# Kernel tuning notes

Measured on AMD Instinct MI355X. Metric: run time of the kernel, lower is better.

Reference implementation:

```python
import jax, jax.numpy as jnp
import numpy as np

N0, N1, N2 = 16000, 12000, 6000
K0, K1 = 10, 5
H, OUT = 256, 128
VOCABS = [50000, 1000, 200]
EDIMS = [64, 32, 32]
EIN = sum(EDIMS)  # 128 input to fc_input


def setup_inputs() -> dict:
    key = jax.random.key(0)
    ks = jax.random.split(key, 40)
    inp = {}
    cols = [jax.random.randint(ks[i], (N0, 1), 0, VOCABS[i]) for i in range(3)]
    inp['x'] = jnp.concatenate(cols, axis=1)
    inp['idx_sim0'] = jax.random.randint(ks[3], (N1, K0), 0, N0)
    inp['idx_cor0'] = jax.random.randint(ks[4], (N1, K0), 0, N0)
    inp['idx_sim1'] = jax.random.randint(ks[5], (N2, K1), 0, N1)
    inp['idx_cor1'] = jax.random.randint(ks[6], (N2, K1), 0, N1)
    k = 7
    for m in ['sim', 'cor']:
        for i in range(3):
            inp[f'emb{i}_{m}'] = jax.random.normal(ks[k], (VOCABS[i], EDIMS[i]), jnp.float32) * 0.02; k += 1
        inp[f'Win_{m}'] = jax.random.normal(ks[k], (EIN, H), jnp.float32) * (1.0 / np.sqrt(EIN)); k += 1
        inp[f'bin_{m}'] = jnp.zeros((H,), jnp.float32)
        inp[f'Wout_{m}'] = jax.random.normal(ks[k], (H, OUT), jnp.float32) * (1.0 / np.sqrt(H)); k += 1
        inp[f'bout_{m}'] = jnp.zeros((OUT,), jnp.float32)
    inp['Ws2c'] = jax.random.normal(ks[k], (OUT, OUT), jnp.float32) * (1.0 / np.sqrt(OUT)); k += 1
    inp['Wc2s'] = jax.random.normal(ks[k], (OUT, OUT), jnp.float32) * (1.0 / np.sqrt(OUT)); k += 1
    inp['a1'] = jnp.array([0.3], jnp.float32)
    inp['a2'] = jnp.array([0.25], jnp.float32)
    inp['b2'] = jnp.array([0.2], jnp.float32)
    return inp


def _coattention(D, Q):
    # D, Q: [N, K, H]
    L = jnp.einsum('nkh,nmh->nkm', D, Q)          # [N, K, K]
    AC = jax.nn.softmax(L, axis=-1)
    AS = jax.nn.softmax(jnp.swapaxes(L, 1, 2), axis=-1)
    CQ = jnp.einsum('nkm,nmh->nkh', AC, Q)        # [N, K, H]
    CD = jnp.einsum('nkm,nmh->nkh', AS, jnp.concatenate([D, CQ], axis=-1))  # [N, K, 2H]
    return jnp.concatenate([Q, CD], axis=-1)       # [N, K, 3H]


def _coagg(feat, idx_sim, idx_cor, mode, n_dst):
    # gather neighbor features per dst node (feat_src[in_edges_id])
    if mode == 'cor':
        D, Q = feat[idx_sim], feat[idx_cor]
    else:
        D, Q = feat[idx_cor], feat[idx_sim]
    h = _coattention(D, Q)                         # [n_dst, K, 3H]
    n, k, f = h.shape
    # AvgPool1d(kernel=3, stride=3) over feature axis -> [n_dst, K, H]
    pooled = h.reshape(n, k, f // 3, 3).mean(axis=-1)
    neigh = pooled.mean(axis=1)                    # mean over neighbors -> [n_dst, H]
    return feat[:n_dst] + neigh


def _branch(x, e0, e1, e2, Win, bin_, Wout, bout, i_s0, i_c0, i_s1, i_c1, mode):
    e = jnp.concatenate([e0[x[:, 0]], e1[x[:, 1]], e2[x[:, 2]]], axis=1)  # [N0, 128]
    h = e @ Win + bin_                             # [N0, H]
    h = jax.nn.relu(_coagg(h, i_s0, i_c0, mode, N1))
    h = _coagg(h, i_s1, i_c1, mode, N2)
    return h @ Wout + bout                         # [N2, OUT]


def reference(x, idx_sim0, idx_cor0, idx_sim1, idx_cor1,
              emb0_sim, emb1_sim, emb2_sim, Win_sim, bin_sim, Wout_sim, bout_sim,
              emb0_cor, emb1_cor, emb2_cor, Win_cor, bin_cor, Wout_cor, bout_cor,
              Ws2c, Wc2s, a1, a2, b2):
    sim = _branch(x, emb0_sim, emb1_sim, emb2_sim, Win_sim, bin_sim, Wout_sim, bout_sim,
                  idx_sim0, idx_cor0, idx_sim1, idx_cor1, 'sim')
    cor = _branch(x, emb0_cor, emb1_cor, emb2_cor, Win_cor, bin_cor, Wout_cor, bout_cor,
                  idx_sim0, idx_cor0, idx_sim1, idx_cor1, 'cor')
    # SemanticIntegration
    z1sim = (1 - a1) * sim + a1 * (cor @ Wc2s)
    z1cor = (1 - a1) * cor + a1 * (sim @ Ws2c)
    z2sim = (1 - a2 - b2) * sim + a2 * (cor @ Wc2s) + b2 * (z1cor @ Wc2s)
    z2cor = (1 - a2 - b2) * cor + a2 * (sim @ Ws2c) + b2 * (z1sim @ Ws2c)
    return jnp.stack([z2sim, z2cor])               # [2, N2, OUT]
```

## Files before the change

### kernel.cpp

```cpp
#include <hip/hip_runtime.h>

#define CH 256

template <int CTRL>
__device__ __forceinline__ float dppAdd(float v) {
    const int m = __builtin_amdgcn_update_dpp(0, __builtin_bit_cast(int, v), CTRL, 0xf, 0xf, true);
    return v + __builtin_bit_cast(float, m);
}

#define OPAQUE4(v) asm volatile("" : "+v"((v).x), "+v"((v).y), "+v"((v).z), "+v"((v).w))

__global__ __launch_bounds__(256) void embed_fc2_kernel(
    const int* __restrict__ x,
    const float* __restrict__ e0a, const float* __restrict__ e1a, const float* __restrict__ e2a,
    const float* __restrict__ Wina, const float* __restrict__ bina, float* __restrict__ h0a,
    const float* __restrict__ e0b, const float* __restrict__ e1b, const float* __restrict__ e2b,
    const float* __restrict__ Winb, const float* __restrict__ binb, float* __restrict__ h0b,
    const int blocksPer)
{
    __shared__ __align__(16) float eT[128][32];
    int bid = blockIdx.x;
    const float *e0, *e1, *e2, *Win, *bin;
    float* h0;
    if (bid < blocksPer) { e0 = e0a; e1 = e1a; e2 = e2a; Win = Wina; bin = bina; h0 = h0a; }
    else { bid -= blocksPer; e0 = e0b; e1 = e1b; e2 = e2b; Win = Winb; bin = binb; h0 = h0b; }

    const int row0 = bid * 32;
    const int t = threadIdx.x;
    const int w = t >> 6, l = t & 63;
    const int r = l & 31;
    const int kcBase = 2 * w + (l >> 5);

#pragma unroll
    for (int j = 0; j < 4; ++j) {
        const int kc = kcBase + 8 * j;
        const int k0 = kc * 4;
        const int row = row0 + r;
        float4 v;
        if (kc < 16)      v = *(const float4*)(e0 + (size_t)x[row * 3 + 0] * 64 + k0);
        else if (kc < 24) v = *(const float4*)(e1 + (size_t)x[row * 3 + 1] * 32 + (k0 - 64));
        else              v = *(const float4*)(e2 + (size_t)x[row * 3 + 2] * 32 + (k0 - 96));
        eT[k0 + 0][r] = v.x; eT[k0 + 1][r] = v.y; eT[k0 + 2][r] = v.z; eT[k0 + 3][r] = v.w;
    }
    __syncthreads();

    const float4 bb = *(const float4*)(bin + l * 4);
    float acc[8][4];
#pragma unroll
    for (int rr = 0; rr < 8; ++rr) {
        acc[rr][0] = bb.x; acc[rr][1] = bb.y; acc[rr][2] = bb.z; acc[rr][3] = bb.w;
    }
#pragma unroll 4
    for (int k = 0; k < 128; ++k) {
        const float4 wv = *(const float4*)(Win + (size_t)k * 256 + l * 4);
        const float4 ea = *(const float4*)&eT[k][w * 8];
        const float4 eb = *(const float4*)&eT[k][w * 8 + 4];
        const float ev[8] = {ea.x, ea.y, ea.z, ea.w, eb.x, eb.y, eb.z, eb.w};
#pragma unroll
        for (int rr = 0; rr < 8; ++rr) {
            acc[rr][0] += ev[rr] * wv.x; acc[rr][1] += ev[rr] * wv.y;
            acc[rr][2] += ev[rr] * wv.z; acc[rr][3] += ev[rr] * wv.w;
        }
    }
#pragma unroll
    for (int rr = 0; rr < 8; ++rr) {
        float4 o = make_float4(acc[rr][0], acc[rr][1], acc[rr][2], acc[rr][3]);
        *(float4*)(h0 + (size_t)(row0 + w * 8 + rr) * 256 + l * 4) = o;
    }
}

template <int KD, int MODE>
__global__ __launch_bounds__(128) void gemm16_kernel(
    const float* __restrict__ ina, const float* __restrict__ Wa,
    const float* __restrict__ auxa, const float* __restrict__ aux2a, float* __restrict__ oa,
    const float* __restrict__ inb, const float* __restrict__ Wb,
    const float* __restrict__ auxb, const float* __restrict__ aux2b, float* __restrict__ ob,
    const int blocksPer, const int nRows,
    const float* __restrict__ a1p, const float* __restrict__ a2p, const float* __restrict__ b2p)
{
    __shared__ __align__(16) float inT[KD][16];
    int bid = blockIdx.x;
    const float *in, *W, *aux, *aux2; float* outp;
    if (bid < blocksPer) { in = ina; W = Wa; aux = auxa; aux2 = aux2a; outp = oa; }
    else { bid -= blocksPer; in = inb; W = Wb; aux = auxb; aux2 = aux2b; outp = ob; }

    const int row0 = bid * 16;
    const int t = threadIdx.x;
    const int row = t & 15;
    const int kc0 = t >> 4;

#pragma unroll
    for (int j = 0; j < KD / 32; ++j) {
        const int kc = kc0 + 8 * j;
        const int k0 = kc * 4;
        int r = row0 + row;
        if (r >= nRows) r = nRows - 1;
        const float4 v = *(const float4*)(in + (size_t)r * KD + k0);
        inT[k0 + 0][row] = v.x; inT[k0 + 1][row] = v.y;
        inT[k0 + 2][row] = v.z; inT[k0 + 3][row] = v.w;
    }
    __syncthreads();

    const int w = t >> 6, l = t & 63;
    const int rg = w * 2 + (l >> 5);
    const int r0 = rg * 4;
    const int cc0 = (l & 31) * 4;

    float acc[4][4];
    if constexpr (MODE == 0) {
        const float4 bb = *(const float4*)(aux + cc0);
#pragma unroll
        for (int rr = 0; rr < 4; ++rr) {
            acc[rr][0] = bb.x; acc[rr][1] = bb.y; acc[rr][2] = bb.z; acc[rr][3] = bb.w;
        }
    } else {
#pragma unroll
        for (int rr = 0; rr < 4; ++rr) acc[rr][0] = acc[rr][1] = acc[rr][2] = acc[rr][3] = 0.f;
    }

#pragma unroll 4
    for (int k = 0; k < KD; ++k) {
        const float4 wv = *(const float4*)(W + (size_t)k * 128 + cc0);
        const float4 ea = *(const float4*)&inT[k][r0];
        const float ev[4] = {ea.x, ea.y, ea.z, ea.w};
#pragma unroll
        for (int rr = 0; rr < 4; ++rr) {
            acc[rr][0] += ev[rr] * wv.x; acc[rr][1] += ev[rr] * wv.y;
            acc[rr][2] += ev[rr] * wv.z; acc[rr][3] += ev[rr] * wv.w;
        }
    }

    float c0 = 0.f, c1 = 0.f, c2 = 0.f;
    if constexpr (MODE == 1) {
        const float a1 = *a1p, a2 = *a2p, b2 = *b2p;
        c0 = 1.f - a2 - b2;
        c1 = a2 + b2 * (1.f - a1);
        c2 = b2 * a1;
    }

#pragma unroll
    for (int rr = 0; rr < 4; ++rr) {
        const int r = row0 + r0 + rr;
        if (r < nRows) {
            float4 o = make_float4(acc[rr][0], acc[rr][1], acc[rr][2], acc[rr][3]);
            if constexpr (MODE == 1) {
                const size_t idx = (size_t)r * 128 + cc0;
                const float4 b1v = *(const float4*)(aux + idx);
                const float4 b2v = *(const float4*)(aux2 + idx);
                o.x = c0 * b1v.x + c1 * b2v.x + c2 * o.x;
                o.y = c0 * b1v.y + c1 * b2v.y + c2 * o.y;
                o.z = c0 * b1v.z + c1 * b2v.z + c2 * o.z;
                o.w = c0 * b1v.w + c1 * b2v.w + c2 * o.w;
            }
            *(float4*)(outp + (size_t)r * 128 + cc0) = o;
        }
    }
}

template <int K>
__global__ __launch_bounds__(256, 2) void coagg_kernel(
    const float* __restrict__ fa, const int* __restrict__ iDa, const int* __restrict__ iQa,
    float* __restrict__ oa,
    const float* __restrict__ fb, const int* __restrict__ iDb, const int* __restrict__ iQb,
    float* __restrict__ ob,
    const int nPer, const int relu)
{
    __shared__ float sL[4][K][K];
    __shared__ float sAC[4][K][K];
    __shared__ float sAS[4][K][K];
    __shared__ float sw_[4][K], su_[4][K];
    __shared__ __align__(16) float sHsum[4][768];

    const int t = threadIdx.x;
    const int wv = t >> 6, lane = t & 63;
    int n = blockIdx.x * 4 + wv;

    const float* feat; const int* idxD; const int* idxQ; float* outp;
    if (n < nPer) { feat = fa; idxD = iDa; idxQ = iQa; outp = oa; }
    else { n -= nPer; feat = fb; idxD = iDb; idxQ = iQb; outp = ob; }

    const float4* fp = (const float4*)feat;

    float4 d[K], q[K];
#pragma unroll
    for (int k = 0; k < K; ++k) {
        const int rD = idxD[n * K + k];
        const int rQ = idxQ[n * K + k];
        d[k] = fp[(size_t)rD * 64 + lane];
        q[k] = fp[(size_t)rQ * 64 + lane];
    }
    const float4 resid = fp[(size_t)n * 64 + lane];
#pragma unroll
    for (int k = 0; k < K; ++k) { OPAQUE4(d[k]); OPAQUE4(q[k]); }

#pragma unroll
    for (int k = 0; k < K; ++k) {
        const float4 dd = d[k];
#pragma unroll
        for (int m0 = 0; m0 < K; m0 += 4) {
            const float4 q0 = q[m0];
            float s0 = dd.x * q0.x + dd.y * q0.y + dd.z * q0.z + dd.w * q0.w;
            float s1 = 0.f, s2 = 0.f, s3 = 0.f;
            if (m0 + 1 < K) {
                const float4 qq = q[(m0 + 1 < K) ? m0 + 1 : 0];
                s1 = dd.x * qq.x + dd.y * qq.y + dd.z * qq.z + dd.w * qq.w;
            }
            if (m0 + 2 < K) {
                const float4 qq = q[(m0 + 2 < K) ? m0 + 2 : 0];
                s2 = dd.x * qq.x + dd.y * qq.y + dd.z * qq.z + dd.w * qq.w;
            }
            if (m0 + 3 < K) {
                const float4 qq = q[(m0 + 3 < K) ? m0 + 3 : 0];
                s3 = dd.x * qq.x + dd.y * qq.y + dd.z * qq.z + dd.w * qq.w;
            }
            asm volatile("v_permlane32_swap_b32 %0, %1" : "+v"(s0), "+v"(s1));
            float a = s0 + s1;
            asm volatile("v_permlane32_swap_b32 %0, %1" : "+v"(s2), "+v"(s3));
            float b = s2 + s3;
            asm volatile("v_permlane16_swap_b32 %0, %1" : "+v"(a), "+v"(b));
            float r = a + b;
            r = dppAdd<0x111>(r);
            r = dppAdd<0x112>(r);
            r = dppAdd<0x114>(r);
            r = dppAdd<0x118>(r);
            const int rowid = lane >> 4;
            const int mm = m0 + (((rowid & 1) << 1) | (rowid >> 1));
            if ((lane & 15) == 15 && mm < K) sL[wv][k][mm] = r;
        }
    }

    if (lane < K) {
        float e_[K], mx = -1e30f;
#pragma unroll
        for (int m = 0; m < K; ++m) mx = fmaxf(mx, sL[wv][lane][m]);
        float ssum = 0.f;
#pragma unroll
        for (int m = 0; m < K; ++m) { e_[m] = __expf(sL[wv][lane][m] - mx); ssum += e_[m]; }
        const float inv = 1.f / ssum;
#pragma unroll
        for (int m = 0; m < K; ++m) sAC[wv][lane][m] = e_[m] * inv;
    }
    {
        const int c = lane - 16;
        if (c >= 0 && c < K) {
            float e_[K], mx = -1e30f;
#pragma unroll
            for (int m = 0; m < K; ++m) mx = fmaxf(mx, sL[wv][m][c]);
            float ssum = 0.f;
#pragma unroll
            for (int m = 0; m < K; ++m) { e_[m] = __expf(sL[wv][m][c] - mx); ssum += e_[m]; }
            const float inv = 1.f / ssum;
#pragma unroll
            for (int m = 0; m < K; ++m) sAS[wv][c][m] = e_[m] * inv;
        }
    }
    {
        const int m2 = lane - 32;
        if (m2 >= 0 && m2 < K) {
            float s = 0.f;
#pragma unroll
            for (int k2 = 0; k2 < K; ++k2) s += sAS[wv][k2][m2];
            sw_[wv][m2] = s;
        }
    }
    {
        const int j2 = lane - 48;
        if (j2 >= 0 && j2 < K) {
            float s = 0.f;
#pragma unroll
            for (int m = 0; m < K; ++m) s += sw_[wv][m] * sAC[wv][m][j2];
            su_[wv][j2] = s;
        }
    }

    float4 h0v = make_float4(0.f, 0.f, 0.f, 0.f);
    float4 h1v = make_float4(0.f, 0.f, 0.f, 0.f);
    float4 h2v = make_float4(0.f, 0.f, 0.f, 0.f);
#pragma unroll
    for (int kx = 0; kx < K; ++kx) {
        const float wk = sw_[wv][kx];
        const float uk = su_[wv][kx];
        const float4 qq = q[kx];
        const float4 dd = d[kx];
        h0v.x += qq.x;      h0v.y += qq.y;      h0v.z += qq.z;      h0v.w += qq.w;
        h1v.x += wk * dd.x; h1v.y += wk * dd.y; h1v.z += wk * dd.z; h1v.w += wk * dd.w;
        h2v.x += uk * qq.x; h2v.y += uk * qq.y; h2v.z += uk * qq.z; h2v.w += uk * qq.w;
    }
    ((float4*)&sHsum[wv][0])[lane]       = h0v;
    ((float4*)&sHsum[wv][0])[64 + lane]  = h1v;
    ((float4*)&sHsum[wv][0])[128 + lane] = h2v;

    float ov[4];
#pragma unroll
    for (int i = 0; i < 4; ++i) {
        const int f = lane * 4 + i;
        ov[i] = (sHsum[wv][3 * f] + sHsum[wv][3 * f + 1] + sHsum[wv][3 * f + 2])
                * (1.0f / (3.0f * K));
    }
    float4 o = make_float4(resid.x + ov[0], resid.y + ov[1],
                           resid.z + ov[2], resid.w + ov[3]);
    if (relu) {
        o.x = fmaxf(o.x, 0.f); o.y = fmaxf(o.y, 0.f);
        o.z = fmaxf(o.z, 0.f); o.w = fmaxf(o.w, 0.f);
    }
    ((float4*)outp)[(size_t)n * 64 + lane] = o;
}

extern "C" void kernel_launch(void* const* d_in, const int* in_sizes, int n_in,
                              void* d_out, int out_size, void* d_ws, size_t ws_size,
                              hipStream_t stream)
{
    const int* x        = (const int*)d_in[0];
    const int* idx_sim0 = (const int*)d_in[1];
    const int* idx_cor0 = (const int*)d_in[2];
    const int* idx_sim1 = (const int*)d_in[3];
    const int* idx_cor1 = (const int*)d_in[4];
    const float* e0s  = (const float*)d_in[5];
    const float* e1s  = (const float*)d_in[6];
    const float* e2s  = (const float*)d_in[7];
    const float* Wins = (const float*)d_in[8];
    const float* bins = (const float*)d_in[9];
    const float* Wouts= (const float*)d_in[10];
    const float* bouts= (const float*)d_in[11];
    const float* e0c  = (const float*)d_in[12];
    const float* e1c  = (const float*)d_in[13];
    const float* e2c  = (const float*)d_in[14];
    const float* Winc = (const float*)d_in[15];
    const float* binc = (const float*)d_in[16];
    const float* Woutc= (const float*)d_in[17];
    const float* boutc= (const float*)d_in[18];
    const float* Ws2c = (const float*)d_in[19];
    const float* Wc2s = (const float*)d_in[20];
    const float* a1 = (const float*)d_in[21];
    const float* a2 = (const float*)d_in[22];
    const float* b2 = (const float*)d_in[23];

    float* outSim = (float*)d_out;
    float* outCor = outSim + 6000 * 128;

    float* ws = (float*)d_ws;
    const size_t needMerged = (size_t)(2 * 16000 * 256 + 2 * 12000 * 256 + 2 * 6000 * 256 + 4 * 6000 * 128) * 4;
    const bool merged = ws_size >= needMerged;

    const int fcBlocks = 6000 / 16;

    if (merged) {
        float* A0 = ws;
        float* A1 = A0 + 16000 * 256;
        float* B0 = A1 + 16000 * 256;
        float* B1 = B0 + 12000 * 256;
        float* C0 = B1 + 12000 * 256;
        float* C1 = C0 + 6000 * 256;
        float* simO = C1 + 6000 * 256;
        float* corO = simO + 6000 * 128;
        float* P    = corO + 6000 * 128;
        float* S    = P + 6000 * 128;

        embed_fc2_kernel<<<1000, 256, 0, stream>>>(x,
            e0s, e1s, e2s, Wins, bins, A0,
            e0c, e1c, e2c, Winc, binc, A1, 500);
        coagg_kernel<10><<<6000, 256, 0, stream>>>(
            A0, idx_cor0, idx_sim0, B0,
            A1, idx_sim0, idx_cor0, B1, 12000, 1);
        coagg_kernel<5><<<3000, 256, 0, stream>>>(
            B0, idx_cor1, idx_sim1, C0,
            B1, idx_sim1, idx_cor1, C1, 6000, 0);
        gemm16_kernel<256, 0><<<2 * fcBlocks, 128, 0, stream>>>(
            C0, Wouts, bouts, nullptr, simO,
            C1, Woutc, boutc, nullptr, corO, fcBlocks, 6000, a1, a2, b2);
        gemm16_kernel<128, 2><<<2 * fcBlocks, 128, 0, stream>>>(
            corO, Wc2s, nullptr, nullptr, P,
            simO, Ws2c, nullptr, nullptr, S, fcBlocks, 6000, a1, a2, b2);
        gemm16_kernel<128, 1><<<2 * fcBlocks, 128, 0, stream>>>(
            S, Wc2s, simO, P, outSim,
            P, Ws2c, corO, S, outCor, fcBlocks, 6000, a1, a2, b2);
    } else {
        float* A = ws;
        float* B = A + 16000 * 256;
        float* C = B + 12000 * 256;
        float* simO = C + 6000 * 256;
        float* corO = simO + 6000 * 128;
        float* P    = corO + 6000 * 128;
        float* S    = P + 6000 * 128;

        for (int b = 0; b < 2; ++b) {
            const float* e0   = (b == 0) ? e0s : e0c;
            const float* e1   = (b == 0) ? e1s : e1c;
            const float* e2   = (b == 0) ? e2s : e2c;
            const float* Win  = (b == 0) ? Wins : Winc;
            const float* bin  = (b == 0) ? bins : binc;
            const float* Wout = (b == 0) ? Wouts : Woutc;
            const float* bout = (b == 0) ? bouts : boutc;
            const int* iD0 = (b == 0) ? idx_cor0 : idx_sim0;
            const int* iQ0 = (b == 0) ? idx_sim0 : idx_cor0;
            const int* iD1 = (b == 0) ? idx_cor1 : idx_sim1;
            const int* iQ1 = (b == 0) ? idx_sim1 : idx_cor1;
            float* branchOut = (b == 0) ? simO : corO;

            embed_fc2_kernel<<<500, 256, 0, stream>>>(x,
                e0, e1, e2, Win, bin, A,
                e0, e1, e2, Win, bin, A, 500);
            coagg_kernel<10><<<3000, 256, 0, stream>>>(
                A, iD0, iQ0, B, A, iD0, iQ0, B, 12000, 1);
            coagg_kernel<5><<<1500, 256, 0, stream>>>(
                B, iD1, iQ1, C, B, iD1, iQ1, C, 6000, 0);
            gemm16_kernel<256, 0><<<fcBlocks, 128, 0, stream>>>(
                C, Wout, bout, nullptr, branchOut,
                C, Wout, bout, nullptr, branchOut, fcBlocks, 6000, a1, a2, b2);
        }
        gemm16_kernel<128, 2><<<2 * fcBlocks, 128, 0, stream>>>(
            corO, Wc2s, nullptr, nullptr, P,
            simO, Ws2c, nullptr, nullptr, S, fcBlocks, 6000, a1, a2, b2);
        gemm16_kernel<128, 1><<<2 * fcBlocks, 128, 0, stream>>>(
            S, Wc2s, simO, P, outSim,
            P, Ws2c, corO, S, outCor, fcBlocks, 6000, a1, a2, b2);
    }
}
```

Measured before the change: 176.0 us.

## Fold output FC and semantic integration into precomputed combined weight matrices

Algebraically composes Wout with Ws2c/Wc2s and the mixing coefficients into combined 256x128 weight matrices and biases, computed by two small prep kernels. The three tail GEMM launches (output FC, cross projection, final mix) become one fused kernel that reads C0 and C1 once and writes both outputs. This removes the intermediate simO/corO/P/S round trips and two launches, at the cost of two extra tiny launches and different floating-point rounding order.

Measured after the change: 215.3 us. 1.22x slower.

```diff
diff --git a/kernel.cpp b/kernel.cpp
--- a/kernel.cpp
+++ b/kernel.cpp
@@ -154,6 +154,206 @@
             }
             *(float4*)(outp + (size_t)r * 128 + cc0) = o;
         }
+    }
+}
+
+__global__ __launch_bounds__(128) void prep1_kernel(
+    const float* __restrict__ Ws2c, const float* __restrict__ Wc2s,
+    const float* __restrict__ bouts, const float* __restrict__ boutc,
+    float* __restrict__ Msc, float* __restrict__ Mcs,
+    float* __restrict__ vs, float* __restrict__ vc)
+{
+    const int bid = blockIdx.x;
+    const int t = threadIdx.x;
+    if (bid == 16) {
+        float s1 = 0.f, s2 = 0.f;
+        for (int k = 0; k < 128; ++k) {
+            s1 += bouts[k] * Ws2c[k * 128 + t];
+            s2 += boutc[k] * Wc2s[k * 128 + t];
+        }
+        vs[t] = s1; vc[t] = s2;
+        return;
+    }
+    const bool isSc = bid < 8;
+    const float* A = isSc ? Ws2c : Wc2s;
+    const float* W = isSc ? Wc2s : Ws2c;
+    float* out = isSc ? Msc : Mcs;
+    const int row0 = (bid & 7) * 16;
+
+    __shared__ __align__(16) float aT[128][16];
+    const int row = t & 15, kc0 = t >> 4;
+#pragma unroll
+    for (int j = 0; j < 4; ++j) {
+        const int k0 = (kc0 + 8 * j) * 4;
+        const float4 v = *(const float4*)(A + (size_t)(row0 + row) * 128 + k0);
+        aT[k0 + 0][row] = v.x; aT[k0 + 1][row] = v.y;
+        aT[k0 + 2][row] = v.z; aT[k0 + 3][row] = v.w;
+    }
+    __syncthreads();
+    const int w = t >> 6, l = t & 63;
+    const int r0 = (w * 2 + (l >> 5)) * 4;
+    const int cc0 = (l & 31) * 4;
+    float acc[4][4];
+#pragma unroll
+    for (int rr = 0; rr < 4; ++rr) acc[rr][0] = acc[rr][1] = acc[rr][2] = acc[rr][3] = 0.f;
+#pragma unroll 4
+    for (int k = 0; k < 128; ++k) {
+        const float4 wv = *(const float4*)(W + (size_t)k * 128 + cc0);
+        const float4 ea = *(const float4*)&aT[k][r0];
+        const float ev[4] = {ea.x, ea.y, ea.z, ea.w};
+#pragma unroll
+        for (int rr = 0; rr < 4; ++rr) {
+            acc[rr][0] += ev[rr] * wv.x; acc[rr][1] += ev[rr] * wv.y;
+            acc[rr][2] += ev[rr] * wv.z; acc[rr][3] += ev[rr] * wv.w;
+        }
+    }
+#pragma unroll
+    for (int rr = 0; rr < 4; ++rr)
+        *(float4*)(out + (size_t)(row0 + r0 + rr) * 128 + cc0) =
+            make_float4(acc[rr][0], acc[rr][1], acc[rr][2], acc[rr][3]);
+}
+
+__global__ __launch_bounds__(128) void prep2_kernel(
+    const float* __restrict__ Wouts, const float* __restrict__ Woutc,
+    const float* __restrict__ Ws2c, const float* __restrict__ Wc2s,
+    const float* __restrict__ bouts, const float* __restrict__ boutc,
+    const float* __restrict__ Msc, const float* __restrict__ Mcs,
+    const float* __restrict__ vs, const float* __restrict__ vc,
+    const float* __restrict__ a1p, const float* __restrict__ a2p,
+    const float* __restrict__ b2p,
+    float* __restrict__ WAs, float* __restrict__ WBs,
+    float* __restrict__ WAc, float* __restrict__ WBc,
+    float* __restrict__ bs, float* __restrict__ bc)
+{
+    const float a1 = *a1p, a2 = *a2p, b2 = *b2p;
+    const float k0 = 1.f - a2 - b2;
+    const float k1 = a2 + b2 * (1.f - a1);
+    const float k2 = b2 * a1;
+    const int bid = blockIdx.x;
+    const int t = threadIdx.x;
+    if (bid == 64) {
+        float s1 = 0.f, s2 = 0.f;
+        for (int k = 0; k < 128; ++k) {
+            s1 += vs[k] * Wc2s[k * 128 + t];
+            s2 += vc[k] * Ws2c[k * 128 + t];
+        }
+        bs[t] = k0 * bouts[t] + k1 * vc[t] + k2 * s1;
+        bc[t] = k0 * boutc[t] + k1 * vs[t] + k2 * s2;
+        return;
+    }
+    const int task = bid >> 4;
+    const int row0 = (bid & 15) * 16;
+    const float *A, *W; float* out; float alpha; bool addBase;
+    if (task == 0)      { A = Wouts; W = Msc;  out = WAs; alpha = k2; addBase = true; }
+    else if (task == 1) { A = Woutc; W = Mcs;  out = WAc; alpha = k2; addBase = true; }
+    else if (task == 2) { A = Woutc; W = Wc2s; out = WBs; alpha = k1; addBase = false; }
+    else                { A = Wouts; W = Ws2c; out = WBc; alpha = k1; addBase = false; }
+
+    __shared__ __align__(16) float aT[128][16];
+    const int row = t & 15, kc0 = t >> 4;
+#pragma unroll
+    for (int j = 0; j < 4; ++j) {
+        const int k0i = (kc0 + 8 * j) * 4;
+        const float4 v = *(const float4*)(A + (size_t)(row0 + row) * 128 + k0i);
+        aT[k0i + 0][row] = v.x; aT[k0i + 1][row] = v.y;
+        aT[k0i + 2][row] = v.z; aT[k0i + 3][row] = v.w;
+    }
+    __syncthreads();
+    const int w = t >> 6, l = t & 63;
+    const int r0 = (w * 2 + (l >> 5)) * 4;
+    const int cc0 = (l & 31) * 4;
+    float acc[4][4];
+#pragma unroll
+    for (int rr = 0; rr < 4; ++rr) acc[rr][0] = acc[rr][1] = acc[rr][2] = acc[rr][3] = 0.f;
+#pragma unroll 4
+    for (int k = 0; k < 128; ++k) {
+        const float4 wv = *(const float4*)(W + (size_t)k * 128 + cc0);
+        const float4 ea = *(const float4*)&aT[k][r0];
+        const float ev[4] = {ea.x, ea.y, ea.z, ea.w};
+#pragma unroll
+        for (int rr = 0; rr < 4; ++rr) {
+            acc[rr][0] += ev[rr] * wv.x; acc[rr][1] += ev[rr] * wv.y;
+            acc[rr][2] += ev[rr] * wv.z; acc[rr][3] += ev[rr] * wv.w;
+        }
+    }
+#pragma unroll
+    for (int rr = 0; rr < 4; ++rr) {
+        const size_t idx = (size_t)(row0 + r0 + rr) * 128 + cc0;
+        float4 o = make_float4(alpha * acc[rr][0], alpha * acc[rr][1],
+                               alpha * acc[rr][2], alpha * acc[rr][3]);
+        if (addBase) {
+            const float4 av = *(const float4*)(A + idx);
+            o.x += k0 * av.x; o.y += k0 * av.y; o.z += k0 * av.z; o.w += k0 * av.w;
+        }
+        *(float4*)(out + idx) = o;
+    }
+}
+
+__global__ __launch_bounds__(128) void outfused_kernel(
+    const float* __restrict__ C0, const float* __restrict__ C1,
+    const float* __restrict__ WAs, const float* __restrict__ WBs,
+    const float* __restrict__ WAc, const float* __restrict__ WBc,
+    const float* __restrict__ bs, const float* __restrict__ bc,
+    float* __restrict__ outSim, float* __restrict__ outCor)
+{
+    __shared__ __align__(16) float c0T[256][16];
+    __shared__ __align__(16) float c1T[256][16];
+    const int t = threadIdx.x;
+    const int row0 = blockIdx.x * 16;
+    const int row = t & 15, kc0 = t >> 4;
+#pragma unroll
+    for (int j = 0; j < 8; ++j) {
+        const int k0i = (kc0 + 8 * j) * 4;
+        float4 v = *(const float4*)(C0 + (size_t)(row0 + row) * 256 + k0i);
+        c0T[k0i + 0][row] = v.x; c0T[k0i + 1][row] = v.y;
+        c0T[k0i + 2][row] = v.z; c0T[k0i + 3][row] = v.w;
+        v = *(const float4*)(C1 + (size_t)(row0 + row) * 256 + k0i);
+        c1T[k0i + 0][row] = v.x; c1T[k0i + 1][row] = v.y;
+        c1T[k0i + 2][row] = v.z; c1T[k0i + 3][row] = v.w;
+    }
+    __syncthreads();
+
+    const int w = t >> 6, l = t & 63;
+    const int r0 = (w * 2 + (l >> 5)) * 4;
+    const int cc0 = (l & 31) * 4;
+
+    float aS[4][4], aC[4][4];
+#pragma unroll
+    for (int rr = 0; rr < 4; ++rr) {
+        aS[rr][0] = aS[rr][1] = aS[rr][2] = aS[rr][3] = 0.f;
+        aC[rr][0] = aC[rr][1] = aC[rr][2] = aC[rr][3] = 0.f;
+    }
+#pragma unroll 2
+    for (int k = 0; k < 256; ++k) {
+        const float4 w1 = *(const float4*)(WAs + (size_t)k * 128 + cc0);
+        const float4 w2 = *(const float4*)(WBs + (size_t)k * 128 + cc0);
+        const float4 w3 = *(const float4*)(WAc + (size_t)k * 128 + cc0);
+        const float4 w4 = *(const float4*)(WBc + (size_t)k * 128 + cc0);
+        const float4 e0 = *(const float4*)&c0T[k][r0];
+        const float4 e1 = *(const float4*)&c1T[k][r0];
+        const float a0[4] = {e0.x, e0.y, e0.z, e0.w};
+        const float b0[4] = {e1.x, e1.y, e1.z, e1.w};
+#pragma unroll
+        for (int rr = 0; rr < 4; ++rr) {
+            aS[rr][0] += a0[rr] * w1.x + b0[rr] * w2.x;
+            aS[rr][1] += a0[rr] * w1.y + b0[rr] * w2.y;
+            aS[rr][2] += a0[rr] * w1.z + b0[rr] * w2.z;
+            aS[rr][3] += a0[rr] * w1.w + b0[rr] * w2.w;
+            aC[rr][0] += b0[rr] * w3.x + a0[rr] * w4.x;
+            aC[rr][1] += b0[rr] * w3.y + a0[rr] * w4.y;
+            aC[rr][2] += b0[rr] * w3.z + a0[rr] * w4.z;
+            aC[rr][3] += b0[rr] * w3.w + a0[rr] * w4.w;
+        }
+    }
+    const float4 bsv = *(const float4*)(bs + cc0);
+    const float4 bcv = *(const float4*)(bc + cc0);
+#pragma unroll
+    for (int rr = 0; rr < 4; ++rr) {
+        const size_t idx = (size_t)(row0 + r0 + rr) * 128 + cc0;
+        *(float4*)(outSim + idx) = make_float4(aS[rr][0] + bsv.x, aS[rr][1] + bsv.y,
+                                               aS[rr][2] + bsv.z, aS[rr][3] + bsv.w);
+        *(float4*)(outCor + idx) = make_float4(aC[rr][0] + bcv.x, aC[rr][1] + bcv.y,
+                                               aC[rr][2] + bcv.z, aC[rr][3] + bcv.w);
     }
 }
 
@@ -342,8 +542,6 @@
     const size_t needMerged = (size_t)(2 * 16000 * 256 + 2 * 12000 * 256 + 2 * 6000 * 256 + 4 * 6000 * 128) * 4;
     const bool merged = ws_size >= needMerged;
 
-    const int fcBlocks = 6000 / 16;
-
     if (merged) {
         float* A0 = ws;
         float* A1 = A0 + 16000 * 256;
@@ -351,10 +549,21 @@
         float* B1 = B0 + 12000 * 256;
         float* C0 = B1 + 12000 * 256;
         float* C1 = C0 + 6000 * 256;
-        float* simO = C1 + 6000 * 256;
-        float* corO = simO + 6000 * 128;
-        float* P    = corO + 6000 * 128;
-        float* S    = P + 6000 * 128;
+        float* Msc = C1 + 6000 * 256;
+        float* Mcs = Msc + 128 * 128;
+        float* vs  = Mcs + 128 * 128;
+        float* vc  = vs + 128;
+        float* WAs = vc + 128;
+        float* WBs = WAs + 256 * 128;
+        float* WAc = WBs + 256 * 128;
+        float* WBc = WAc + 256 * 128;
+        float* bs  = WBc + 256 * 128;
+        float* bc  = bs + 128;
+
+        prep1_kernel<<<17, 128, 0, stream>>>(Ws2c, Wc2s, bouts, boutc, Msc, Mcs, vs, vc);
+        prep2_kernel<<<65, 128, 0, stream>>>(Wouts, Woutc, Ws2c, Wc2s, bouts, boutc,
+                                             Msc, Mcs, vs, vc, a1, a2, b2,
+                                             WAs, WBs, WAc, WBc, bs, bc);
 
         embed_fc2_kernel<<<1000, 256, 0, stream>>>(x,
             e0s, e1s, e2s, Wins, bins, A0,
@@ -365,15 +574,8 @@
         coagg_kernel<5><<<3000, 256, 0, stream>>>(
             B0, idx_cor1, idx_sim1, C0,
             B1, idx_sim1, idx_cor1, C1, 6000, 0);
-        gemm16_kernel<256, 0><<<2 * fcBlocks, 128, 0, stream>>>(
-            C0, Wouts, bouts, nullptr, simO,
-            C1, Woutc, boutc, nullptr, corO, fcBlocks, 6000, a1, a2, b2);
-        gemm16_kernel<128, 2><<<2 * fcBlocks, 128, 0, stream>>>(
-            corO, Wc2s, nullptr, nullptr, P,
-            simO, Ws2c, nullptr, nullptr, S, fcBlocks, 6000, a1, a2, b2);
-        gemm16_kernel<128, 1><<<2 * fcBlocks, 128, 0, stream>>>(
-            S, Wc2s, simO, P, outSim,
-            P, Ws2c, corO, S, outCor, fcBlocks, 6000, a1, a2, b2);
+        outfused_kernel<<<375, 128, 0, stream>>>(
+            C0, C1, WAs, WBs, WAc, WBc, bs, bc, outSim, outCor);
     } else {
         float* A = ws;
         float* B = A + 16000 * 256;
@@ -382,6 +584,7 @@
         float* corO = simO + 6000 * 128;
         float* P    = corO + 6000 * 128;
         float* S    = P + 6000 * 128;
+        const int fcBlocks = 6000 / 16;
 
         for (int b = 0; b < 2; ++b) {
             const float* e0   = (b == 0) ? e0s : e0c;
```
